# Performance work log

Measured on AMD Instinct MI355X. Metric: run time of the kernel, lower is better.

Reference implementation:

```python
import jax, jax.numpy as jnp
import numpy as np

K = -1.0          # manifold curvature (hyperbolic / Poincare ball)
SK = 1.0          # sqrt(|K|)
EPS = 1e-7


def _artan_k(x):
    # inverse of tan_k for K<0: artanh(sqrt(|K|) x)/sqrt(|K|)
    return jnp.arctanh(jnp.clip(SK * x, -1.0 + EPS, 1.0 - EPS)) / SK


def _tan_k(x):
    return jnp.tanh(SK * x) / SK


def _norm(x):
    return jnp.maximum(jnp.linalg.norm(x, axis=-1, keepdims=True), 1e-15)


def mobius_add(x, y):
    xy = jnp.sum(x * y, -1, keepdims=True)
    x2 = jnp.sum(x * x, -1, keepdims=True)
    y2 = jnp.sum(y * y, -1, keepdims=True)
    num = (1.0 - 2.0 * K * xy - K * y2) * x + (1.0 + K * x2) * y
    den = 1.0 - 2.0 * K * xy + K * K * x2 * y2
    return num / jnp.maximum(den, 1e-15)


def mobius_scalar_mul(r, x):
    # r may be scalar or (n,1) per-row scalar
    xn = _norm(x)
    return _tan_k(r * _artan_k(xn)) * x / xn


def mobius_matvec(W, x):
    # geoopt convention: (m @ x) per point -> x @ W^T
    xn = _norm(x)
    mx = x @ W.T
    mxn = _norm(mx)
    return _tan_k(mxn / xn * _artan_k(xn)) * mx / mxn


def lambda_x(x):
    # conformal factor lambda_x = 2 / (1 + K |x|^2); returns shape (...,)
    return 2.0 / jnp.maximum(1.0 + K * jnp.sum(x * x, -1), 1e-10)


def expmap0(u):
    un = _norm(u)
    return _tan_k(un) * u / un


def logmap0(y):
    yn = _norm(y)
    return _artan_k(yn) * y / yn


def kappa_left_multiply(A, X):
    # Vectorized per-node weighted gyro-midpoint + mobius scalar mul.
    # out_i = (sum_j A_ij) otimes gyromidpoint(X, weights=A_i)
    gamma = lambda_x(X)                              # (n,)
    denom = A @ (gamma - 1.0)                        # (n,)
    denom = jnp.where(jnp.abs(denom) < 1e-10, 1e-10, denom)
    nom = A @ (gamma[:, None] * X)                   # (n,d)
    two_mean = nom / denom[:, None]
    m = mobius_scalar_mul(0.5, two_mean)             # gyromidpoint
    return mobius_scalar_mul(jnp.sum(A, axis=1, keepdims=True), m)


def setup_inputs() -> dict:
    key = jax.random.key(0)
    k1, k2, k3, k4, k5 = jax.random.split(key, 5)
    n, d, c = 8192, 256, 16
    # node embeddings on the Poincare ball (small norm, well inside the ball)
    X = 0.01 * jax.random.normal(k1, (n, d), jnp.float32)
    # dense normalized adjacency (positive weights, row sums O(1))
    A_hat = jax.random.uniform(k2, (n, n), dtype=jnp.float32) / n
    W = jax.random.uniform(k3, (d, d), dtype=jnp.float32)        # torch.rand init
    W_logits = jax.random.uniform(k4, (d, c), dtype=jnp.float32)
    # p_ks = expmap0(rand), scaled for numerical stability
    p_ks = expmap0(0.05 * jax.random.uniform(k5, (c, d), dtype=jnp.float32))
    return {"X": X, "A_hat": A_hat, "W": W, "W_logits": W_logits, "p_ks": p_ks}


def reference(X, A_hat, W, W_logits, p_ks):
    # hidden kappa-GCN layer
    XW = mobius_matvec(W, X)                          # (n,d)
    AXW = kappa_left_multiply(A_hat, XW)              # (n,d)
    H1 = expmap0(jax.nn.relu(logmap0(AXW)))           # manifold.apply(relu)
    # hyperbolic logits (kappa != 0 branch, K<0 -> asinh)
    z = mobius_add(-p_ks[None, :, :], H1[:, None, :]) # (n,k,d)
    z_n = jnp.linalg.norm(z, axis=-1)                 # (n,k)
    a_n = jnp.maximum(jnp.linalg.norm(W_logits, axis=0), 1e-15)  # (k,)
    za = jnp.einsum('nkd,dk->nk', z, W_logits)
    den = jnp.maximum(1.0 + K * z_n * z_n, 1e-10) * a_n
    dist = jnp.arcsinh(2.0 * SK * za / den)
    lam = lambda_x(p_ks)                              # (k,)
    logits = (lam * a_n / SK) * dist                  # (n,k)
    return A_hat @ logits
```

## Files before the change

### kernel.cpp

```cpp
#include <hip/hip_runtime.h>
#include <math.h>

#define Nn 8192
#define Dd 256
#define Cc 16

#define OFF_BP   4194304u
#define OFF_LOG  5242880u
#define OFF_G1B  5373952u
#define OFF_DEN  5378048u
#define OFF_RS   5410816u
#define OFF_KC   5443584u
#define WS_FLOATS 5443648u

typedef short vshort8 __attribute__((ext_vector_type(8)));
typedef float vfloat4 __attribute__((ext_vector_type(4)));

#define AS1 __attribute__((address_space(1)))
#define AS3 __attribute__((address_space(3)))

__device__ __forceinline__ float clip1(float x) {
    return fminf(fmaxf(x, -1.0f + 1e-7f), 1.0f - 1e-7f);
}

__device__ __forceinline__ unsigned short f2bf(float f) {
    unsigned int u = __float_as_uint(f);
    u += 0x7fff + ((u >> 16) & 1);
    return (unsigned short)(u >> 16);
}

__device__ __forceinline__ float bf2f(unsigned short b) {
    return __uint_as_float(((unsigned int)b) << 16);
}

__device__ __forceinline__ float waveReduce(float v) {
    #pragma unroll
    for (int off = 32; off; off >>= 1) v += __shfl_down(v, off);
    return v;
}

__device__ __forceinline__ float blockReduceBcast(float v, float* red) {
    int t = threadIdx.x, w = t >> 6, l = t & 63;
    v = waveReduce(v);
    if (l == 0) red[w] = v;
    __syncthreads();
    if (t == 0) red[0] = red[0] + red[1] + red[2] + red[3];
    __syncthreads();
    float r = red[0];
    __syncthreads();
    return r;
}

__global__ __launch_bounds__(256) void k_consts(const float* __restrict__ Wl,
                                                const float* __restrict__ Pk,
                                                float* __restrict__ kc) {
    __shared__ float red[8];
    int t = threadIdx.x, k = blockIdx.x;
    float pv = Pk[k * Dd + t];
    float wv = Wl[t * Cc + k];
    float p2 = blockReduceBcast(pv * pv, red);
    float pw = blockReduceBcast(pv * wv, red);
    float w2 = blockReduceBcast(wv * wv, red);
    if (t == 0) {
        float an  = fmaxf(sqrtf(w2), 1e-15f);
        float lam = 2.0f / fmaxf(1.0f - p2, 1e-10f);
        kc[k * 4 + 0] = p2; kc[k * 4 + 1] = pw;
        kc[k * 4 + 2] = an; kc[k * 4 + 3] = lam;
    }
}

__global__ __launch_bounds__(256) void k_front(const float* __restrict__ X,
                                               const float* __restrict__ W,
                                               unsigned short* __restrict__ Bp,
                                               unsigned short* __restrict__ g1b) {
    __shared__ __align__(16) unsigned short Xs[32][256];
    __shared__ __align__(16) unsigned short Gs[32][258];
    __shared__ float xs2[32];
    __shared__ float scal[32];
    __shared__ float red4[32][4];

    const int t = threadIdx.x;
    const int l = t & 63, w = t >> 6;
    const int ll = l & 15, kh = l >> 4;
    const int m0 = blockIdx.x * 32;
    const int ar = t >> 3, aq = t & 7;
    const int c0 = w * 64;

    float x2p = 0.f;
    #pragma unroll
    for (int tc = 0; tc < 4; ++tc) {
        const float* xp = &X[(size_t)(m0 + ar) * Dd + tc * 64 + aq * 8];
        vfloat4 v0 = *(const vfloat4*)xp;
        vfloat4 v1 = *(const vfloat4*)(xp + 4);
        vshort8 o;
        #pragma unroll
        for (int e = 0; e < 4; ++e) {
            x2p += v0[e] * v0[e] + v1[e] * v1[e];
            o[e] = (short)f2bf(v0[e]);
            o[e + 4] = (short)f2bf(v1[e]);
        }
        int byte = (tc * 64 + aq * 8) * 2;
        *(vshort8*)((char*)&Xs[ar][0] + (byte ^ ((ar & 7) << 4))) = o;
    }
    x2p += __shfl_xor(x2p, 1); x2p += __shfl_xor(x2p, 2); x2p += __shfl_xor(x2p, 4);
    if (aq == 0) xs2[ar] = x2p;
    __syncthreads();

    vfloat4 acc[2][4];
    #pragma unroll
    for (int mi = 0; mi < 2; ++mi)
        #pragma unroll
        for (int ni = 0; ni < 4; ++ni)
            acc[mi][ni] = (vfloat4){0.f, 0.f, 0.f, 0.f};
    #pragma unroll
    for (int tc = 0; tc < 4; ++tc) {
        vshort8 bf[8];
        #pragma unroll
        for (int ni = 0; ni < 4; ++ni)
            #pragma unroll
            for (int kk = 0; kk < 2; ++kk) {
                const float* wp = &W[(size_t)(c0 + ni * 16 + ll) * Dd
                                     + tc * 64 + kh * 8 + kk * 32];
                vfloat4 b0 = *(const vfloat4*)wp;
                vfloat4 b1 = *(const vfloat4*)(wp + 4);
                vshort8 o;
                #pragma unroll
                for (int e = 0; e < 4; ++e) {
                    o[e] = (short)f2bf(b0[e]);
                    o[e + 4] = (short)f2bf(b1[e]);
                }
                bf[ni * 2 + kk] = o;
            }
        #pragma unroll
        for (int kk = 0; kk < 2; ++kk) {
            int byte = (tc * 64 + kh * 8 + kk * 32) * 2;
            vshort8 af[2];
            #pragma unroll
            for (int mi = 0; mi < 2; ++mi) {
                int row = mi * 16 + ll;
                af[mi] = *(const vshort8*)((const char*)&Xs[row][0]
                                           + (byte ^ ((row & 7) << 4)));
            }
            #pragma unroll
            for (int mi = 0; mi < 2; ++mi)
                #pragma unroll
                for (int ni = 0; ni < 4; ++ni)
                    acc[mi][ni] = __builtin_amdgcn_mfma_f32_16x16x32_bf16(
                        af[mi], bf[ni * 2 + kk], acc[mi][ni], 0, 0, 0);
        }
    }

    #pragma unroll
    for (int mi = 0; mi < 2; ++mi)
        #pragma unroll
        for (int j = 0; j < 4; ++j) {
            float p = 0.f;
            #pragma unroll
            for (int ni = 0; ni < 4; ++ni)
                p += acc[mi][ni][j] * acc[mi][ni][j];
            p += __shfl_xor(p, 1); p += __shfl_xor(p, 2);
            p += __shfl_xor(p, 4); p += __shfl_xor(p, 8);
            if (ll == 0) red4[mi * 16 + kh * 4 + j][w] = p;
        }
    __syncthreads();

    if (t < 32) {
        float mx2 = red4[t][0] + red4[t][1] + red4[t][2] + red4[t][3];
        float xn = fmaxf(sqrtf(xs2[t]), 1e-15f);
        float mxn = fmaxf(sqrtf(mx2), 1e-15f);
        float s = tanhf(mxn / xn * atanhf(clip1(xn))) / mxn;
        float xw2 = s * s * mx2;
        float gamma = 2.0f / fmaxf(1.0f - xw2, 1e-10f);
        scal[t] = gamma * s;
        g1b[m0 + t] = f2bf(gamma - 1.0f);
    }
    __syncthreads();

    #pragma unroll
    for (int mi = 0; mi < 2; ++mi)
        #pragma unroll
        for (int ni = 0; ni < 4; ++ni) {
            int row = mi * 16 + kh * 4;
            int col = c0 + ni * 16 + ll;
            #pragma unroll
            for (int j = 0; j < 4; ++j)
                Gs[row + j][col] = f2bf(scal[row + j] * acc[mi][ni][j]);
        }
    __syncthreads();

    const int s = blockIdx.x;
    #pragma unroll
    for (int pass = 0; pass < 4; ++pass) {
        int c = pass * 256 + t;
        int gni = c >> 6, lc = c & 63;
        int col = (gni >> 2) * 64 + (gni & 3) * 16 + (lc & 15);
        int kh8 = (lc >> 4) * 8;
        vshort8 o;
        #pragma unroll
        for (int e = 0; e < 8; ++e) o[e] = (short)Gs[kh8 + e][col];
        *(vshort8*)&Bp[((size_t)(s * 16 + gni) * 64 + lc) * 8] = o;
    }
}

__global__ __launch_bounds__(256, 4) void k_gemm1_mfma(
        const float* __restrict__ A,
        const unsigned short* __restrict__ Bp,
        const unsigned short* __restrict__ g1b,
        unsigned short* __restrict__ Pp,
        float* __restrict__ denp,
        float* __restrict__ rsp) {
    __shared__ __align__(16) float As[2][32 * 128];
    __shared__ __align__(16) unsigned short g1s[2048];

    const int t = threadIdx.x, l = t & 63, w = t >> 6;
    const int id = blockIdx.x;
    const int splt = id & 3;
    const int m0 = (id >> 2) * 32;
    const int kb = splt * 2048;
    const int kh = l >> 4, ll15 = l & 15;

    const float* asrc[4];
    #pragma unroll
    for (int i = 0; i < 4; ++i) {
        int q = w * 256 + i * 64 + l;
        int row = q >> 5, c = q & 31;
        asrc[i] = &A[(size_t)(m0 + row) * Nn + kb + ((c ^ (row & 7)) << 2)];
    }
    const unsigned short* bB = Bp + (size_t)(splt * 1024 + w * 4) * 512 + l * 8;

    vfloat4 acc[2][4];
    #pragma unroll
    for (int mi = 0; mi < 2; ++mi)
        #pragma unroll
        for (int ni = 0; ni < 4; ++ni)
            acc[mi][ni] = (vfloat4){0.f, 0.f, 0.f, 0.f};
    float dacc[2] = {0.f, 0.f}, racc[2] = {0.f, 0.f};

    *(uint4*)&g1s[t * 8] = *(const uint4*)&g1b[kb + t * 8];
    #pragma unroll
    for (int i = 0; i < 4; ++i)
        __builtin_amdgcn_global_load_lds((const AS1 unsigned int*)asrc[i],
            (AS3 unsigned int*)&As[0][w * 1024 + i * 256], 16, 0, 0);
    __syncthreads();

    for (int p = 0; p < 16; ++p) {
        const int cur = p & 1;
        const unsigned short* bp = bB + p * 32768;
        vshort8 bf[8];
        #pragma unroll
        for (int h = 0; h < 2; ++h) {
            #pragma unroll
            for (int s2 = 0; s2 < 2; ++s2)
                #pragma unroll
                for (int ni = 0; ni < 4; ++ni)
                    bf[s2 * 4 + ni] = *(const vshort8*)
                        (bp + ((h * 2 + s2) * 16 + ni) * 512);
            if (h == 0 && p < 15) {
                #pragma unroll
                for (int i = 0; i < 4; ++i)
                    __builtin_amdgcn_global_load_lds(
                        (const AS1 unsigned int*)(asrc[i] + (p + 1) * 128),
                        (AS3 unsigned int*)&As[cur ^ 1][w * 1024 + i * 256],
                        16, 0, 0);
            }
            #pragma unroll
            for (int s2 = 0; s2 < 2; ++s2) {
                const int ss = h * 2 + s2;
                vshort8 gv;
                if (w == 0)
                    gv = *(const vshort8*)&g1s[p * 128 + ss * 32 + kh * 8];
                vshort8 af[2];
                #pragma unroll
                for (int mi = 0; mi < 2; ++mi) {
                    int row = mi * 16 + ll15;
                    int ba = row * 512 + (((ss * 8 + kh * 2) ^ (row & 7)) << 4);
                    vfloat4 v0 = *(const vfloat4*)((const char*)&As[cur][0] + ba);
                    vfloat4 v1 = *(const vfloat4*)((const char*)&As[cur][0] + (ba ^ 16));
                    vshort8 o;
                    #pragma unroll
                    for (int e = 0; e < 4; ++e) {
                        o[e] = (short)f2bf(v0[e]);
                        o[e + 4] = (short)f2bf(v1[e]);
                    }
                    af[mi] = o;
                    if (w == 0) {
                        #pragma unroll
                        for (int e = 0; e < 4; ++e) {
                            dacc[mi] += v0[e] * bf2f((unsigned short)gv[e])
                                      + v1[e] * bf2f((unsigned short)gv[e + 4]);
                            racc[mi] += v0[e] + v1[e];
                        }
                    }
                }
                #pragma unroll
                for (int mi = 0; mi < 2; ++mi)
                    #pragma unroll
                    for (int ni = 0; ni < 4; ++ni)
                        acc[mi][ni] = __builtin_amdgcn_mfma_f32_16x16x32_bf16(
                            af[mi], bf[s2 * 4 + ni], acc[mi][ni], 0, 0, 0);
            }
        }
        __syncthreads();
    }

    if (w == 0) {
        #pragma unroll
        for (int mi = 0; mi < 2; ++mi) {
            dacc[mi] += __shfl_xor(dacc[mi], 16);
            dacc[mi] += __shfl_xor(dacc[mi], 32);
            racc[mi] += __shfl_xor(racc[mi], 16);
            racc[mi] += __shfl_xor(racc[mi], 32);
        }
        if (l < 16) {
            #pragma unroll
            for (int mi = 0; mi < 2; ++mi) {
                denp[splt * Nn + m0 + mi * 16 + l] = dacc[mi];
                rsp [splt * Nn + m0 + mi * 16 + l] = racc[mi];
            }
        }
    }

    unsigned short* P = Pp + (size_t)splt * ((size_t)Nn * Dd);
    #pragma unroll
    for (int mi = 0; mi < 2; ++mi)
        #pragma unroll
        for (int ni = 0; ni < 4; ++ni) {
            int row = m0 + mi * 16 + (kh << 2);
            int col = w * 64 + ni * 16 + ll15;
            #pragma unroll
            for (int j = 0; j < 4; ++j)
                P[(size_t)(row + j) * Dd + col] = f2bf(acc[mi][ni][j]);
        }
}

__global__ __launch_bounds__(256) void k_rowfix(const unsigned short* __restrict__ Pp,
                                                const float* __restrict__ denp,
                                                const float* __restrict__ rsp,
                                                const float* __restrict__ Pk,
                                                const float* __restrict__ Wl,
                                                const float* __restrict__ kc,
                                                float* __restrict__ logits) {
    __shared__ float red[8];
    __shared__ float hs[256];
    __shared__ float PQ[16][2];
    int i = blockIdx.x, t = threadIdx.x;
    float nom = 0.f;
    #pragma unroll
    for (int s = 0; s < 4; ++s)
        nom += bf2f(Pp[(size_t)s * Nn * Dd + (size_t)i * Dd + t]);
    float dv = denp[i] + denp[Nn + i] + denp[2 * Nn + i] + denp[3 * Nn + i];
    dv = (fabsf(dv) < 1e-10f) ? 1e-10f : dv;
    float tm = nom / dv;
    float r2 = blockReduceBcast(tm * tm, red);
    float r = fmaxf(sqrtf(r2), 1e-15f);
    float mmul = tanhf(0.5f * atanhf(clip1(r))) / r;
    float mj = mmul * tm;
    float mn2 = blockReduceBcast(mj * mj, red);
    float mn = fmaxf(sqrtf(mn2), 1e-15f);
    float sA = rsp[i] + rsp[Nn + i] + rsp[2 * Nn + i] + rsp[3 * Nn + i];
    float axmul = tanhf(sA * atanhf(clip1(mn))) / mn;
    float axw = axmul * mj;
    float yn2 = blockReduceBcast(axw * axw, red);
    float yn = fmaxf(sqrtf(yn2), 1e-15f);
    float v = atanhf(clip1(yn)) / yn * axw;
    float u = fmaxf(v, 0.0f);
    float un2 = blockReduceBcast(u * u, red);
    float un = fmaxf(sqrtf(un2), 1e-15f);
    float h = tanhf(un) / un * u;
    float h2 = blockReduceBcast(h * h, red);
    hs[t] = h;
    __syncthreads();
    int w = t >> 6, l = t & 63;
    #pragma unroll
    for (int kk = 0; kk < 4; ++kk) {
        int k = w * 4 + kk;
        float pp = 0.f, qq = 0.f;
        #pragma unroll
        for (int m = 0; m < 4; ++m) {
            float hv = hs[l + 64 * m];
            pp += hv * Pk[k * Dd + l + 64 * m];
            qq += hv * Wl[(l + 64 * m) * Cc + k];
        }
        pp = waveReduce(pp);
        qq = waveReduce(qq);
        if (l == 0) { PQ[k][0] = pp; PQ[k][1] = qq; }
    }
    __syncthreads();
    if (t < 16) {
        int k = t;
        float p2 = kc[k * 4 + 0], pw = kc[k * 4 + 1];
        float an = kc[k * 4 + 2], lam = kc[k * 4 + 3];
        float P = PQ[k][0], Q = PQ[k][1];
        float alpha = 1.0f - 2.0f * P + h2;
        float beta  = 1.0f - p2;
        float Dm = fmaxf(1.0f - 2.0f * P + p2 * h2, 1e-15f);
        float za  = (-alpha * pw + beta * Q) / Dm;
        float zn2 = (alpha * alpha * p2 - 2.0f * alpha * beta * P + beta * beta * h2)
                    / (Dm * Dm);
        float dd = fmaxf(1.0f - zn2, 1e-10f) * an;
        float dist = asinhf(2.0f * za / dd);
        logits[(size_t)i * Cc + k] = lam * an * dist;
    }
}

__global__ __launch_bounds__(256) void k_gemm2(const float* __restrict__ A,
                                               const float* __restrict__ L,
                                               float* __restrict__ part) {
    __shared__ __align__(16) float Ls[64 * 20];
    __shared__ float Pacc[256 * 16];
    int t = threadIdx.x;
    int r0 = blockIdx.x * 256;
    int jbase = blockIdx.y * 512;
    int q = t & 3, g = t >> 2;
    float acc[4][16] = {};
    for (int jc = 0; jc < 512; jc += 64) {
        {
            int jrow = t >> 2, kq = t & 3;
            *(float4*)&Ls[jrow * 20 + kq * 4] =
                *(const float4*)&L[(size_t)(jbase + jc + jrow) * Cc + kq * 4];
        }
        __syncthreads();
        #pragma unroll
        for (int m = 0; m < 4; ++m) {
            int jl = m * 16 + q * 4;
            float av[4][4];
            #pragma unroll
            for (int rr = 0; rr < 4; ++rr) {
                float4 tmp = *(const float4*)&A[(size_t)(r0 + g * 4 + rr) * Nn
                                                + jbase + jc + jl];
                av[rr][0] = tmp.x; av[rr][1] = tmp.y;
                av[rr][2] = tmp.z; av[rr][3] = tmp.w;
            }
            #pragma unroll
            for (int jj = 0; jj < 4; ++jj) {
                const float* lr = &Ls[(jl + jj) * 20];
                float lv[16];
                #pragma unroll
                for (int k2 = 0; k2 < 16; k2 += 4) {
                    float4 lt = *(const float4*)&lr[k2];
                    lv[k2] = lt.x; lv[k2 + 1] = lt.y;
                    lv[k2 + 2] = lt.z; lv[k2 + 3] = lt.w;
                }
                #pragma unroll
                for (int rr = 0; rr < 4; ++rr)
                    #pragma unroll
                    for (int k2 = 0; k2 < 16; ++k2)
                        acc[rr][k2] += av[rr][jj] * lv[k2];
            }
        }
        __syncthreads();
    }
    for (int ii = t; ii < 4096; ii += 256) Pacc[ii] = 0.f;
    __syncthreads();
    for (int qq = 0; qq < 4; ++qq) {
        if (q == qq) {
            #pragma unroll
            for (int rr = 0; rr < 4; ++rr)
                #pragma unroll
                for (int k2 = 0; k2 < 16; ++k2)
                    Pacc[(g * 4 + rr) * 16 + k2] += acc[rr][k2];
        }
        __syncthreads();
    }
    float* dst = &part[(size_t)blockIdx.y * (Nn * Cc) + (size_t)r0 * Cc];
    for (int ii = t * 4; ii < 4096; ii += 1024)
        *(float4*)&dst[ii] = *(const float4*)&Pacc[ii];
}

__global__ __launch_bounds__(256) void k_reduce(const float* __restrict__ part,
                                                float* __restrict__ out) {
    int i = blockIdx.x * 256 + threadIdx.x;
    float s = 0.f;
    #pragma unroll
    for (int j = 0; j < 16; ++j) s += part[(size_t)j * (Nn * Cc) + i];
    out[i] = s;
}

extern "C" void kernel_launch(void* const* d_in, const int* in_sizes, int n_in,
                              void* d_out, int out_size, void* d_ws, size_t ws_size,
                              hipStream_t stream) {
    const float* X  = (const float*)d_in[0];
    const float* A  = (const float*)d_in[1];
    const float* W  = (const float*)d_in[2];
    const float* Wl = (const float*)d_in[3];
    const float* Pk = (const float*)d_in[4];
    float* out = (float*)d_out;
    float* ws = (float*)d_ws;
    if (ws_size < (size_t)WS_FLOATS * sizeof(float)) return;

    unsigned short* Pp  = (unsigned short*)ws;
    float* part = ws;
    unsigned short* Bp  = (unsigned short*)(ws + OFF_BP);
    float* lg   = ws + OFF_LOG;
    unsigned short* g1b = (unsigned short*)(ws + OFF_G1B);
    float* denp = ws + OFF_DEN;
    float* rsp  = ws + OFF_RS;
    float* kc   = ws + OFF_KC;

    k_consts<<<16, 256, 0, stream>>>(Wl, Pk, kc);
    k_front<<<256, 256, 0, stream>>>(X, W, Bp, g1b);
    k_gemm1_mfma<<<1024, 256, 0, stream>>>(A, Bp, g1b, Pp, denp, rsp);
    k_rowfix<<<Nn, 256, 0, stream>>>(Pp, denp, rsp, Pk, Wl, kc, lg);
    k_gemm2<<<dim3(32, 16), 256, 0, stream>>>(A, lg, part);
    k_reduce<<<512, 256, 0, stream>>>(part, out);
}
```

Measured before the change: 228.6 us.

## Restructure gemm1 with 64-row tiles, 4-stage A pipeline and LDS-staged B

Doubles the gemm1 block's M tile from 32 to 64 rows and halves the grid, which cuts how often each block re-reads the B operand per output row. The k loop moves to 32-wide slabs. A is fetched through a 4-deep LDS ring and B is now staged through a double-buffered LDS copy using async global_load_lds. Explicit vmcnt waits and raw s_barrier calls replace __syncthreads so loads stay in flight across iterations. The costs are higher register and LDS use (launch bounds drop to 2 blocks per CU) and fragile hand-written wait counts.

```diff
diff --git a/kernel.cpp b/kernel.cpp
--- a/kernel.cpp
+++ b/kernel.cpp
@@ -202,110 +202,150 @@
     }
 }
 
-__global__ __launch_bounds__(256, 4) void k_gemm1_mfma(
+__device__ __forceinline__ void g1_issueB(const unsigned short* __restrict__ Bp,
+        unsigned short (&Bs)[2][16][512], int bbuf, int splt, int slab,
+        int w, int l) {
+    #pragma unroll
+    for (int ni = 0; ni < 4; ++ni)
+        __builtin_amdgcn_global_load_lds(
+            (const AS1 unsigned int*)
+                (Bp + ((size_t)((splt * 64 + slab) * 16 + w * 4 + ni) * 512) + l * 8),
+            (AS3 unsigned int*)&Bs[bbuf][w * 4 + ni][0], 16, 0, 0);
+}
+
+__device__ __forceinline__ void g1_issueA(const float* const (&asrc)[2],
+        float (&As)[4][2048], int buf, int w, int tile) {
+    #pragma unroll
+    for (int i = 0; i < 2; ++i)
+        __builtin_amdgcn_global_load_lds(
+            (const AS1 unsigned int*)(asrc[i] + tile * 32),
+            (AS3 unsigned int*)&As[buf][i * 1024 + w * 256], 16, 0, 0);
+}
+
+__device__ __forceinline__ void g1_phase(const float (&As)[4][2048],
+        const unsigned short (&Bs)[2][16][512], const unsigned short* g1s,
+        int cur, int bbuf, int p, int w, int kh, int ll15, int l,
+        vfloat4 (&acc)[4][4], float (&dacc)[4], float (&racc)[4]) {
+    vshort8 gv = {};
+    if (w == 0) gv = *(const vshort8*)&g1s[p * 32 + kh * 8];
+    vshort8 bf[4];
+    #pragma unroll
+    for (int ni = 0; ni < 4; ++ni)
+        bf[ni] = *(const vshort8*)&Bs[bbuf][w * 4 + ni][l * 8];
+    vshort8 af[4];
+    #pragma unroll
+    for (int mi = 0; mi < 4; ++mi) {
+        int row = mi * 16 + ll15;
+        int ba = row * 128 + (((kh * 2) ^ (row & 7)) << 4);
+        vfloat4 v0 = *(const vfloat4*)((const char*)&As[cur][0] + ba);
+        vfloat4 v1 = *(const vfloat4*)((const char*)&As[cur][0] + (ba ^ 16));
+        vshort8 o;
+        #pragma unroll
+        for (int e = 0; e < 4; ++e) {
+            o[e] = (short)f2bf(v0[e]);
+            o[e + 4] = (short)f2bf(v1[e]);
+        }
+        af[mi] = o;
+        if (w == 0) {
+            #pragma unroll
+            for (int e = 0; e < 4; ++e) {
+                dacc[mi] += v0[e] * bf2f((unsigned short)gv[e])
+                          + v1[e] * bf2f((unsigned short)gv[e + 4]);
+                racc[mi] += v0[e] + v1[e];
+            }
+        }
+    }
+    #pragma unroll
+    for (int mi = 0; mi < 4; ++mi)
+        #pragma unroll
+        for (int ni = 0; ni < 4; ++ni)
+            acc[mi][ni] = __builtin_amdgcn_mfma_f32_16x16x32_bf16(
+                af[mi], bf[ni], acc[mi][ni], 0, 0, 0);
+}
+
+__global__ __launch_bounds__(256, 2) void k_gemm1_mfma(
         const float* __restrict__ A,
         const unsigned short* __restrict__ Bp,
         const unsigned short* __restrict__ g1b,
         unsigned short* __restrict__ Pp,
         float* __restrict__ denp,
         float* __restrict__ rsp) {
-    __shared__ __align__(16) float As[2][32 * 128];
+    __shared__ __align__(16) float As[4][2048];
+    __shared__ __align__(16) unsigned short Bs[2][16][512];
     __shared__ __align__(16) unsigned short g1s[2048];
 
     const int t = threadIdx.x, l = t & 63, w = t >> 6;
     const int id = blockIdx.x;
     const int splt = id & 3;
-    const int m0 = (id >> 2) * 32;
+    const int m0 = (id >> 2) * 64;
     const int kb = splt * 2048;
     const int kh = l >> 4, ll15 = l & 15;
 
-    const float* asrc[4];
-    #pragma unroll
-    for (int i = 0; i < 4; ++i) {
-        int q = w * 256 + i * 64 + l;
-        int row = q >> 5, c = q & 31;
+    const float* asrc[2];
+    #pragma unroll
+    for (int i = 0; i < 2; ++i) {
+        int q = i * 256 + t;
+        int row = q >> 3, c = q & 7;
         asrc[i] = &A[(size_t)(m0 + row) * Nn + kb + ((c ^ (row & 7)) << 2)];
     }
-    const unsigned short* bB = Bp + (size_t)(splt * 1024 + w * 4) * 512 + l * 8;
-
-    vfloat4 acc[2][4];
-    #pragma unroll
-    for (int mi = 0; mi < 2; ++mi)
+
+    vfloat4 acc[4][4];
+    #pragma unroll
+    for (int mi = 0; mi < 4; ++mi)
         #pragma unroll
         for (int ni = 0; ni < 4; ++ni)
             acc[mi][ni] = (vfloat4){0.f, 0.f, 0.f, 0.f};
-    float dacc[2] = {0.f, 0.f}, racc[2] = {0.f, 0.f};
-
-    *(uint4*)&g1s[t * 8] = *(const uint4*)&g1b[kb + t * 8];
-    #pragma unroll
-    for (int i = 0; i < 4; ++i)
-        __builtin_amdgcn_global_load_lds((const AS1 unsigned int*)asrc[i],
-            (AS3 unsigned int*)&As[0][w * 1024 + i * 256], 16, 0, 0);
-    __syncthreads();
-
-    for (int p = 0; p < 16; ++p) {
-        const int cur = p & 1;
-        const unsigned short* bp = bB + p * 32768;
-        vshort8 bf[8];
-        #pragma unroll
-        for (int h = 0; h < 2; ++h) {
-            #pragma unroll
-            for (int s2 = 0; s2 < 2; ++s2)
-                #pragma unroll
-                for (int ni = 0; ni < 4; ++ni)
-                    bf[s2 * 4 + ni] = *(const vshort8*)
-                        (bp + ((h * 2 + s2) * 16 + ni) * 512);
-            if (h == 0 && p < 15) {
-                #pragma unroll
-                for (int i = 0; i < 4; ++i)
-                    __builtin_amdgcn_global_load_lds(
-                        (const AS1 unsigned int*)(asrc[i] + (p + 1) * 128),
-                        (AS3 unsigned int*)&As[cur ^ 1][w * 1024 + i * 256],
-                        16, 0, 0);
-            }
-            #pragma unroll
-            for (int s2 = 0; s2 < 2; ++s2) {
-                const int ss = h * 2 + s2;
-                vshort8 gv;
-                if (w == 0)
-                    gv = *(const vshort8*)&g1s[p * 128 + ss * 32 + kh * 8];
-                vshort8 af[2];
-                #pragma unroll
-                for (int mi = 0; mi < 2; ++mi) {
-                    int row = mi * 16 + ll15;
-                    int ba = row * 512 + (((ss * 8 + kh * 2) ^ (row & 7)) << 4);
-                    vfloat4 v0 = *(const vfloat4*)((const char*)&As[cur][0] + ba);
-                    vfloat4 v1 = *(const vfloat4*)((const char*)&As[cur][0] + (ba ^ 16));
-                    vshort8 o;
-                    #pragma unroll
-                    for (int e = 0; e < 4; ++e) {
-                        o[e] = (short)f2bf(v0[e]);
-                        o[e + 4] = (short)f2bf(v1[e]);
-                    }
-                    af[mi] = o;
-                    if (w == 0) {
-                        #pragma unroll
-                        for (int e = 0; e < 4; ++e) {
-                            dacc[mi] += v0[e] * bf2f((unsigned short)gv[e])
-                                      + v1[e] * bf2f((unsigned short)gv[e + 4]);
-                            racc[mi] += v0[e] + v1[e];
-                        }
-                    }
-                }
-                #pragma unroll
-                for (int mi = 0; mi < 2; ++mi)
-                    #pragma unroll
-                    for (int ni = 0; ni < 4; ++ni)
-                        acc[mi][ni] = __builtin_amdgcn_mfma_f32_16x16x32_bf16(
-                            af[mi], bf[s2 * 4 + ni], acc[mi][ni], 0, 0, 0);
-            }
-        }
-        __syncthreads();
-    }
+    float dacc[4] = {0.f, 0.f, 0.f, 0.f}, racc[4] = {0.f, 0.f, 0.f, 0.f};
+
+    {
+        uint4 g1v = *(const uint4*)&g1b[kb + t * 8];
+        *(uint4*)&g1s[t * 8] = g1v;
+        g1_issueB(Bp, Bs, 0, splt, 0, w, l);
+        g1_issueA(asrc, As, 0, w, 0);
+        g1_issueA(asrc, As, 1, w, 1);
+        g1_issueA(asrc, As, 2, w, 2);
+        asm volatile("s_waitcnt vmcnt(4) lgkmcnt(0)" ::: "memory");
+        __builtin_amdgcn_s_barrier();
+        __builtin_amdgcn_sched_barrier(0);
+    }
+
+    for (int u = 0; u < 15; ++u) {
+        #pragma unroll
+        for (int pp = 0; pp < 4; ++pp) {
+            const int p = u * 4 + pp;
+            g1_issueB(Bp, Bs, (pp & 1) ^ 1, splt, p + 1, w, l);
+            g1_issueA(asrc, As, (pp + 3) & 3, w, p + 3);
+            asm volatile("s_waitcnt vmcnt(8)" ::: "memory");
+            g1_phase(As, Bs, g1s, pp, pp & 1, p, w, kh, ll15, l, acc, dacc, racc);
+            __builtin_amdgcn_s_barrier();
+            __builtin_amdgcn_sched_barrier(0);
+        }
+    }
+    g1_issueB(Bp, Bs, 1, splt, 61, w, l);
+    g1_issueA(asrc, As, 3, w, 63);
+    asm volatile("s_waitcnt vmcnt(8)" ::: "memory");
+    g1_phase(As, Bs, g1s, 0, 0, 60, w, kh, ll15, l, acc, dacc, racc);
+    __builtin_amdgcn_s_barrier();
+    __builtin_amdgcn_sched_barrier(0);
+
+    g1_issueB(Bp, Bs, 0, splt, 62, w, l);
+    asm volatile("s_waitcnt vmcnt(6)" ::: "memory");
+    g1_phase(As, Bs, g1s, 1, 1, 61, w, kh, ll15, l, acc, dacc, racc);
+    __builtin_amdgcn_s_barrier();
+    __builtin_amdgcn_sched_barrier(0);
+
+    g1_issueB(Bp, Bs, 1, splt, 63, w, l);
+    asm volatile("s_waitcnt vmcnt(4)" ::: "memory");
+    g1_phase(As, Bs, g1s, 2, 0, 62, w, kh, ll15, l, acc, dacc, racc);
+    __builtin_amdgcn_s_barrier();
+    __builtin_amdgcn_sched_barrier(0);
+
+    asm volatile("s_waitcnt vmcnt(0)" ::: "memory");
+    g1_phase(As, Bs, g1s, 3, 1, 63, w, kh, ll15, l, acc, dacc, racc);
 
     if (w == 0) {
         #pragma unroll
-        for (int mi = 0; mi < 2; ++mi) {
+        for (int mi = 0; mi < 4; ++mi) {
             dacc[mi] += __shfl_xor(dacc[mi], 16);
             dacc[mi] += __shfl_xor(dacc[mi], 32);
             racc[mi] += __shfl_xor(racc[mi], 16);
@@ -313,7 +353,7 @@
         }
         if (l < 16) {
             #pragma unroll
-            for (int mi = 0; mi < 2; ++mi) {
+            for (int mi = 0; mi < 4; ++mi) {
                 denp[splt * Nn + m0 + mi * 16 + l] = dacc[mi];
                 rsp [splt * Nn + m0 + mi * 16 + l] = racc[mi];
             }
@@ -322,7 +362,7 @@
 
     unsigned short* P = Pp + (size_t)splt * ((size_t)Nn * Dd);
     #pragma unroll
-    for (int mi = 0; mi < 2; ++mi)
+    for (int mi = 0; mi < 4; ++mi)
         #pragma unroll
         for (int ni = 0; ni < 4; ++ni) {
             int row = m0 + mi * 16 + (kh << 2);
@@ -499,7 +539,7 @@
 
     k_consts<<<16, 256, 0, stream>>>(Wl, Pk, kc);
     k_front<<<256, 256, 0, stream>>>(X, W, Bp, g1b);
-    k_gemm1_mfma<<<1024, 256, 0, stream>>>(A, Bp, g1b, Pp, denp, rsp);
+    k_gemm1_mfma<<<512, 256, 0, stream>>>(A, Bp, g1b, Pp, denp, rsp);
     k_rowfix<<<Nn, 256, 0, stream>>>(Pp, denp, rsp, Pk, Wl, kc, lg);
     k_gemm2<<<dim3(32, 16), 256, 0, stream>>>(A, lg, part);
     k_reduce<<<512, 256, 0, stream>>>(part, out);
```

Result: slower. 235.9 us (+3.2%).
